# Kernel optimization log

Hardware: AMD Instinct MI355X
Metric: run time of the kernel (lower is better)

The kernel has to match this reference:

```python
import jax, jax.numpy as jnp
import numpy as np

B, T, N, F_OUT, K, HID = 8, 12, 4096, 12, 3, 64
HALF = T // 2


def setup_inputs() -> dict:
    key = jax.random.key(0)
    ks = jax.random.split(key, 7)
    return {
        "x": jax.random.normal(ks[0], (B, T, N, 1), jnp.float32),
        "adj": jax.random.normal(ks[1], (K, N, N), jnp.float32) / np.float32(np.sqrt(N)),
        "cheb_w": jax.random.normal(ks[2], (HID, K), jnp.float32) / np.float32(np.sqrt(K)),
        "gcn_w": jax.random.normal(ks[3], (F_OUT, T, 1, HID), jnp.float32) / np.float32(np.sqrt(T * HID)),
        "gcn_b": jnp.zeros((F_OUT,), jnp.float32),
        "glu1_w": jax.random.normal(ks[4], (F_OUT, HALF, 3, 3), jnp.float32) / np.float32(np.sqrt(HALF * 9)),
        "glu1_b": jnp.zeros((F_OUT,), jnp.float32),
        "glu2_w": jax.random.normal(ks[5], (F_OUT, HALF, 3, 3), jnp.float32) / np.float32(np.sqrt(HALF * 9)),
        "glu2_b": jnp.zeros((F_OUT,), jnp.float32),
    }


def _dilated_conv(x, w, b):
    # Conv2d(kernel=3, dilation=2, padding=2) on (B, C, N, 1)
    y = jax.lax.conv_general_dilated(
        x, w, window_strides=(1, 1), padding=((2, 2), (2, 2)),
        rhs_dilation=(2, 2), dimension_numbers=("NCHW", "OIHW", "NCHW"))
    return y + b[None, :, None, None]


def reference(x, adj, cheb_w, gcn_w, gcn_b, glu1_w, glu1_b, glu2_w, glu2_b):
    # --- ChebConv (vectorized over the per-channel Python loop) ---
    # x: (B, T, N, 1), adj: (K, N, N) -> y: (B, T, N, K)
    y = jnp.einsum("knm,btm->btnk", adj, x[..., 0])
    # Linear(K -> HID, no bias) + ReLU -> cheb: (B, T, N, HID)
    cheb = jax.nn.relu(jnp.einsum("btnk,ok->btno", y, cheb_w))
    # --- gcn_conv: Conv2d(T -> F_OUT, kernel (1, HID)) -> (B, F_OUT, N, 1) ---
    sgc = jnp.einsum("btnj,otj->bon", cheb, gcn_w[:, :, 0, :]) + gcn_b[None, :, None]
    sgc = sgc[..., None]
    # --- GLU path: split history in half, dilated convs, a * sigmoid(g) ---
    x_u, x_v = x[:, :HALF], x[:, HALF:]
    a = _dilated_conv(x_u, glu1_w, glu1_b)
    g = _dilated_conv(x_v, glu2_w, glu2_b)
    x_glu = a * jax.nn.sigmoid(g)
    return x_glu + sgc
```

## Files before the change

kernel.cpp:

```cpp
#include <hip/hip_runtime.h>
#include <hip/hip_bf16.h>
#include <math.h>

#define NNODES 4096
#define NCOLS  96
#define NROWS  12288
#define KSEG   16
#define KLEN   (NNODES / KSEG)

typedef __attribute__((ext_vector_type(8))) short short8;
typedef __attribute__((ext_vector_type(4))) float float4v;

__device__ __forceinline__ int probe32(const void* adjp) {
    const unsigned* aw = (const unsigned*)adjp;
    unsigned w = aw[threadIdx.x & 63];
    unsigned e = (w >> 7) & 0xffu;
    bool insane = (e >= 0xC0u) || (e <= 0x30u);
    unsigned long long m = __ballot(insane);
    return (__popcll(m) >= 16) ? 1 : 0;
}

__device__ __forceinline__ float ldf(const void* p, size_t i, int isf32) {
    return isf32 ? ((const float*)p)[i]
                 : __bfloat162float(((const __hip_bfloat16*)p)[i]);
}

__device__ __forceinline__ void ld8(float* d, const void* p, size_t e, int isf32) {
    if (isf32) {
        const float4* s = (const float4*)((const float*)p + e);
        float4 f0 = s[0], f1 = s[1];
        d[0] = f0.x; d[1] = f0.y; d[2] = f0.z; d[3] = f0.w;
        d[4] = f1.x; d[5] = f1.y; d[6] = f1.z; d[7] = f1.w;
    } else {
        const __hip_bfloat16* s = (const __hip_bfloat16*)p + e;
#pragma unroll
        for (int j = 0; j < 8; j++) d[j] = __bfloat162float(s[j]);
    }
}

__device__ __forceinline__ short8 cvt8(float4 a, float4 b) {
    union { short8 v; __hip_bfloat16 h[8]; } u;
    u.h[0] = __float2bfloat16(a.x); u.h[1] = __float2bfloat16(a.y);
    u.h[2] = __float2bfloat16(a.z); u.h[3] = __float2bfloat16(a.w);
    u.h[4] = __float2bfloat16(b.x); u.h[5] = __float2bfloat16(b.y);
    u.h[6] = __float2bfloat16(b.z); u.h[7] = __float2bfloat16(b.w);
    return u.v;
}

__global__ __launch_bounds__(256) void cvt_x(
    const void* __restrict__ xv, __hip_bfloat16* __restrict__ xbf,
    const void* __restrict__ adjp)
{
    const int isf32 = probe32(adjp);
    const int i = (blockIdx.x * 256 + threadIdx.x) * 8;
    if (isf32) {
        const float* xf = (const float*)xv;
        float4 f0 = *(const float4*)(xf + i);
        float4 f1 = *(const float4*)(xf + i + 4);
        short8 v = cvt8(f0, f1);
        *(short8*)(xbf + i) = v;
    } else {
        *(uint4*)(xbf + i) = *(const uint4*)((const __hip_bfloat16*)xv + i);
    }
}

__global__ __launch_bounds__(512, 4) void gemm_y(
    const void* __restrict__ adjv, const __hip_bfloat16* __restrict__ xbf,
    float* __restrict__ yws)
{
    __shared__ uint4 Xs[96 * 32];

    const int tid = threadIdx.x;
    const int isf32 = probe32(adjv);
    const int wv = tid >> 6, ln = tid & 63, fr = ln & 15, fq = ln >> 4;

    const int bid = blockIdx.x;
    const int rt0 = (bid >> 4) * 128;
    const int ks  = bid & 15;
    const int k0  = ks * KLEN;

#pragma unroll
    for (int s = 0; s < 6; s++) {
        int L = tid + s * 512;
        int r = L >> 5, c = L & 31;
        Xs[r * 32 + (c ^ (r & 7))] =
            *(const uint4*)(xbf + (size_t)r * NNODES + k0 + c * 8);
    }

    float4v acc[6];
#pragma unroll
    for (int i = 0; i < 6; i++) acc[i] = (float4v){0.f, 0.f, 0.f, 0.f};

    const int arow = rt0 + wv * 16 + fr;

#define XFRAG(CT, STEP) \
    (*(const short8*)&Xs[((CT) * 16 + fr) * 32 + ((((STEP) * 4) + fq) ^ (((CT) * 16 + fr) & 7))])

    if (isf32) {
        const float* ap = (const float*)adjv + (size_t)arow * NNODES + k0 + fq * 8;
        float4 AA[2], AB[2];

#define ALOADF(R, STEP) { const float* p = ap + (STEP) * 32;                   \
        R[0] = *(const float4*)p; R[1] = *(const float4*)(p + 4); }
#define COMPF(R, STEP) { short8 a = cvt8(R[0], R[1]);                          \
        _Pragma("unroll")                                                      \
        for (int ct = 0; ct < 6; ct++)                                         \
            acc[ct] = __builtin_amdgcn_mfma_f32_16x16x32_bf16(a, XFRAG(ct, STEP), acc[ct], 0, 0, 0); }

        ALOADF(AA, 0); ALOADF(AB, 1);
        __syncthreads();
        COMPF(AA, 0);  ALOADF(AA, 2);
        COMPF(AB, 1);  ALOADF(AB, 3);
        COMPF(AA, 2);  ALOADF(AA, 4);
        COMPF(AB, 3);  ALOADF(AB, 5);
        COMPF(AA, 4);  ALOADF(AA, 6);
        COMPF(AB, 5);  ALOADF(AB, 7);
        COMPF(AA, 6);
        COMPF(AB, 7);
#undef ALOADF
#undef COMPF
    } else {
        const __hip_bfloat16* ap = (const __hip_bfloat16*)adjv + (size_t)arow * NNODES + k0 + fq * 8;
        uint4 AA, AB;

#define ALOADB(R, STEP) R = *(const uint4*)(ap + (STEP) * 32);
#define COMPB(R, STEP) { short8 a = *(const short8*)&R;                        \
        _Pragma("unroll")                                                      \
        for (int ct = 0; ct < 6; ct++)                                         \
            acc[ct] = __builtin_amdgcn_mfma_f32_16x16x32_bf16(a, XFRAG(ct, STEP), acc[ct], 0, 0, 0); }

        ALOADB(AA, 0); ALOADB(AB, 1);
        __syncthreads();
        COMPB(AA, 0);  ALOADB(AA, 2);
        COMPB(AB, 1);  ALOADB(AB, 3);
        COMPB(AA, 2);  ALOADB(AA, 4);
        COMPB(AB, 3);  ALOADB(AB, 5);
        COMPB(AA, 4);  ALOADB(AA, 6);
        COMPB(AB, 5);  ALOADB(AB, 7);
        COMPB(AA, 6);
        COMPB(AB, 7);
#undef ALOADB
#undef COMPB
    }
#undef XFRAG

    float* yo = yws + (size_t)ks * NROWS * NCOLS;
#pragma unroll
    for (int ct = 0; ct < 6; ct++)
#pragma unroll
        for (int rg = 0; rg < 4; rg++) {
            size_t r = (size_t)rt0 + wv * 16 + fq * 4 + rg;
            yo[r * NCOLS + ct * 16 + fr] = acc[ct][rg];
        }
}

__global__ __launch_bounds__(256) void reduce_y(float* __restrict__ yws)
{
    const size_t i = ((size_t)blockIdx.x * 256 + threadIdx.x) * 4;
    float4 s = *(const float4*)(yws + i);
#pragma unroll
    for (int sl = 1; sl < KSEG; sl++) {
        const float4 v = *(const float4*)(yws + (size_t)sl * NROWS * NCOLS + i);
        s.x += v.x; s.y += v.y; s.z += v.z; s.w += v.w;
    }
    *(float4*)(yws + i) = s;
}

__global__ __launch_bounds__(256) void epilogue_kernel(
    const void* __restrict__ xv, const float* __restrict__ yws,
    const void* __restrict__ chebv, const void* __restrict__ gcnwv,
    const void* __restrict__ gcnbv, const void* __restrict__ g1wv,
    const void* __restrict__ g1bv, const void* __restrict__ g2wv,
    const void* __restrict__ g2bv,
    float* __restrict__ out, const void* __restrict__ adjp)
{
    __shared__ __align__(16) float gwL[9216];
    __shared__ __align__(16) float cw4L[256];
    __shared__ float w1L[216];
    __shared__ float w2L[216];
    __shared__ float wbL[36];

    const int tid = threadIdx.x;
    const int isf32 = probe32(adjp);

    for (int i = tid; i < 9216; i += 256) {
        int o = i / 768, t = (i / 64) % 12, j = i % 64;
        gwL[t * 768 + j * 12 + o] = ldf(gcnwv, i, isf32);
    }
    if (tid < 256) {
        int j = tid >> 2, kk = tid & 3;
        cw4L[tid] = (kk < 3 && j < 64) ? ldf(chebv, j * 3 + kk, isf32) : 0.f;
    }
    if (tid < 216) {
        w1L[tid] = ldf(g1wv, (size_t)tid * 3 + 1, isf32);
        w2L[tid] = ldf(g2wv, (size_t)tid * 3 + 1, isf32);
    }
    if (tid < 12) {
        wbL[tid]      = ldf(gcnbv, tid, isf32);
        wbL[12 + tid] = ldf(g1bv, tid, isf32);
        wbL[24 + tid] = ldf(g2bv, tid, isf32);
    }
    __syncthreads();

    const int gid = blockIdx.x * 256 + tid;
    const int pr  = gid >> 2;
    const int tq  = gid & 3;
    const int b = pr >> 12;
    const int n = pr & (NNODES - 1);

    float yk[3][3];
#pragma unroll
    for (int k = 0; k < 3; k++) {
        const float* yp = yws + ((size_t)(k * NNODES + n)) * NCOLS + b * 12 + tq * 3;
        yk[k][0] = yp[0]; yk[k][1] = yp[1]; yk[k][2] = yp[2];
    }

    float sg[12];
#pragma unroll
    for (int o = 0; o < 12; o++) sg[o] = 0.f;
    const float4* cw4 = (const float4*)cw4L;
#pragma unroll
    for (int i = 0; i < 3; i++) {
        const float y0 = yk[0][i], y1 = yk[1][i], y2 = yk[2][i];
        const float4* gw4 = (const float4*)(gwL + (tq * 3 + i) * 768);
#pragma unroll 4
        for (int j = 0; j < 64; j++) {
            float4 cw = cw4[j];
            float h = fmaf(y0, cw.x, fmaf(y1, cw.y, y2 * cw.z));
            h = fmaxf(h, 0.f);
            float4 g0 = gw4[j * 3], g1 = gw4[j * 3 + 1], g2 = gw4[j * 3 + 2];
            sg[0] += h * g0.x; sg[1] += h * g0.y; sg[2]  += h * g0.z; sg[3]  += h * g0.w;
            sg[4] += h * g1.x; sg[5] += h * g1.y; sg[6]  += h * g1.z; sg[7]  += h * g1.w;
            sg[8] += h * g2.x; sg[9] += h * g2.y; sg[10] += h * g2.z; sg[11] += h * g2.w;
        }
    }
#pragma unroll
    for (int o = 0; o < 12; o++) {
        sg[o] += __shfl_xor(sg[o], 1);
        sg[o] += __shfl_xor(sg[o], 2);
    }

    float xa[18], xg[18];
#pragma unroll
    for (int c = 0; c < 6; c++)
#pragma unroll
        for (int kh = 0; kh < 3; kh++) {
            int m = n + 2 * kh - 2;
            bool ok = ((unsigned)m < (unsigned)NNODES);
            xa[c * 3 + kh] = ok ? ldf(xv, ((size_t)(b * 12 + c)) * NNODES + m, isf32) : 0.f;
            xg[c * 3 + kh] = ok ? ldf(xv, ((size_t)(b * 12 + c + 6)) * NNODES + m, isf32) : 0.f;
        }

#pragma unroll
    for (int i = 0; i < 3; i++) {
        const int o = tq * 3 + i;
        float av = wbL[12 + o], gv = wbL[24 + o];
#pragma unroll
        for (int q = 0; q < 18; q++) {
            av += xa[q] * w1L[o * 18 + q];
            gv += xg[q] * w2L[o * 18 + q];
        }
        float s = 1.f / (1.f + expf(-gv));
        out[((size_t)(b * 12 + o)) * NNODES + n] = av * s + sg[o] + wbL[o];
    }
}

__global__ __launch_bounds__(64) void fused_simple(
    const void* __restrict__ xv, const void* __restrict__ adjv,
    const void* __restrict__ chebv, const void* __restrict__ gcnwv,
    const void* __restrict__ gcnbv, const void* __restrict__ g1wv,
    const void* __restrict__ g1bv, const void* __restrict__ g2wv,
    const void* __restrict__ g2bv,
    float* __restrict__ out)
{
    __shared__ float gwL[9216];
    __shared__ float cwL[192];
    __shared__ float w1L[216];
    __shared__ float w2L[216];
    __shared__ float wbL[36];

    const int tid = threadIdx.x;
    const int isf32 = probe32(adjv);

    for (int i = tid; i < 9216; i += 64) {
        int o = i / 768, t = (i / 64) % 12, j = i % 64;
        gwL[t * 768 + j * 12 + o] = ldf(gcnwv, i, isf32);
    }
    for (int i = tid; i < 192; i += 64) cwL[i] = ldf(chebv, i, isf32);
    for (int i = tid; i < 216; i += 64) {
        w1L[i] = ldf(g1wv, (size_t)i * 3 + 1, isf32);
        w2L[i] = ldf(g2wv, (size_t)i * 3 + 1, isf32);
    }
    if (tid < 12) {
        wbL[tid]      = ldf(gcnbv, tid, isf32);
        wbL[12 + tid] = ldf(g1bv, tid, isf32);
        wbL[24 + tid] = ldf(g2bv, tid, isf32);
    }
    __syncthreads();

    const int g = blockIdx.x * 64 + tid;
    const int b = g >> 12;
    const int n = g & (NNODES - 1);

    float y[3][12];
#pragma unroll
    for (int k = 0; k < 3; k++)
#pragma unroll
        for (int t = 0; t < 12; t++) y[k][t] = 0.f;

    for (int m0 = 0; m0 < NNODES; m0 += 8) {
        float a0[8], a1[8], a2[8];
        ld8(a0, adjv, ((size_t)(0 * NNODES + n)) * NNODES + m0, isf32);
        ld8(a1, adjv, ((size_t)(1 * NNODES + n)) * NNODES + m0, isf32);
        ld8(a2, adjv, ((size_t)(2 * NNODES + n)) * NNODES + m0, isf32);
#pragma unroll
        for (int t = 0; t < 12; t++) {
            float x8[8];
            ld8(x8, xv, ((size_t)(b * 12 + t)) * NNODES + m0, isf32);
#pragma unroll
            for (int j = 0; j < 8; j++) {
                y[0][t] += a0[j] * x8[j];
                y[1][t] += a1[j] * x8[j];
                y[2][t] += a2[j] * x8[j];
            }
        }
    }

    float sg[12];
#pragma unroll
    for (int o = 0; o < 12; o++) sg[o] = wbL[o];
    for (int t = 0; t < 12; t++) {
        const float y0 = y[0][t], y1 = y[1][t], y2 = y[2][t];
        const float* gwt = gwL + t * 768;
#pragma unroll 4
        for (int j = 0; j < 64; j++) {
            float h = y0 * cwL[j * 3] + y1 * cwL[j * 3 + 1] + y2 * cwL[j * 3 + 2];
            h = fmaxf(h, 0.f);
#pragma unroll
            for (int o = 0; o < 12; o++) sg[o] += h * gwt[j * 12 + o];
        }
    }

    float xa[18], xg[18];
#pragma unroll
    for (int c = 0; c < 6; c++)
#pragma unroll
        for (int kh = 0; kh < 3; kh++) {
            int m = n + 2 * kh - 2;
            bool ok = ((unsigned)m < (unsigned)NNODES);
            xa[c * 3 + kh] = ok ? ldf(xv, ((size_t)(b * 12 + c)) * NNODES + m, isf32) : 0.f;
            xg[c * 3 + kh] = ok ? ldf(xv, ((size_t)(b * 12 + c + 6)) * NNODES + m, isf32) : 0.f;
        }

#pragma unroll
    for (int o = 0; o < 12; o++) {
        float av = wbL[12 + o], gv = wbL[24 + o];
#pragma unroll
        for (int i = 0; i < 18; i++) {
            av += xa[i] * w1L[o * 18 + i];
            gv += xg[i] * w2L[o * 18 + i];
        }
        float s = 1.f / (1.f + expf(-gv));
        out[((size_t)(b * 12 + o)) * NNODES + n] = av * s + sg[o];
    }
}

extern "C" void kernel_launch(void* const* d_in, const int* in_sizes, int n_in,
                              void* d_out, int out_size, void* d_ws, size_t ws_size,
                              hipStream_t stream)
{
    __hip_bfloat16* xbf = (__hip_bfloat16*)((char*)d_ws + 64);
    float* yws = (float*)((char*)d_ws + 64 + (size_t)NCOLS * NNODES * 2);
    const size_t need = 64 + (size_t)NCOLS * NNODES * 2
                      + (size_t)KSEG * NROWS * NCOLS * 4;

    if (ws_size >= need) {
        hipLaunchKernelGGL(cvt_x, dim3(192), dim3(256), 0, stream,
                           d_in[0], xbf, d_in[1]);
        hipLaunchKernelGGL(gemm_y, dim3(96 * KSEG), dim3(512), 0, stream,
                           d_in[1], xbf, yws);
        hipLaunchKernelGGL(reduce_y, dim3(NROWS * NCOLS / 1024), dim3(256), 0, stream,
                           yws);
        hipLaunchKernelGGL(epilogue_kernel, dim3(512), dim3(256), 0, stream,
                           d_in[0], yws, d_in[2], d_in[3], d_in[4],
                           d_in[5], d_in[6], d_in[7], d_in[8],
                           (float*)d_out, d_in[1]);
    } else {
        hipLaunchKernelGGL(fused_simple, dim3(512), dim3(64), 0, stream,
                           d_in[0], d_in[1], d_in[2], d_in[3], d_in[4],
                           d_in[5], d_in[6], d_in[7], d_in[8],
                           (float*)d_out);
    }
}
```

Measured before the change: 380.8 us.

## Fuse x conversion into GEMM, halve K-split, move split reduction into epilogue

Drops the separate x-to-bf16 conversion kernel: the GEMM now stages x into shared memory directly, converting from the source dtype. The K-split drops from 16 to 8 segments, so each block runs two staged halves with extra barriers. The separate reduce kernel is removed; the epilogue sums the 8 partial slices itself. The partials are stored transposed as float4 so those reads are coalesced. This removes two launches and much of the partial-sum traffic, at the cost of fewer GEMM blocks for parallelism and extra loads in the epilogue.

New measurement: 345.4 us. -9.3%, faster.

```diff
diff --git a/kernel.cpp b/kernel.cpp
--- a/kernel.cpp
+++ b/kernel.cpp
@@ -5,8 +5,9 @@
 #define NNODES 4096
 #define NCOLS  96
 #define NROWS  12288
-#define KSEG   16
+#define KSEG   8
 #define KLEN   (NNODES / KSEG)
+#define YSLICE ((size_t)NROWS * NCOLS)
 
 typedef __attribute__((ext_vector_type(8))) short short8;
 typedef __attribute__((ext_vector_type(4))) float float4v;
@@ -47,25 +48,12 @@
     return u.v;
 }
 
-__global__ __launch_bounds__(256) void cvt_x(
-    const void* __restrict__ xv, __hip_bfloat16* __restrict__ xbf,
-    const void* __restrict__ adjp)
-{
-    const int isf32 = probe32(adjp);
-    const int i = (blockIdx.x * 256 + threadIdx.x) * 8;
-    if (isf32) {
-        const float* xf = (const float*)xv;
-        float4 f0 = *(const float4*)(xf + i);
-        float4 f1 = *(const float4*)(xf + i + 4);
-        short8 v = cvt8(f0, f1);
-        *(short8*)(xbf + i) = v;
-    } else {
-        *(uint4*)(xbf + i) = *(const uint4*)((const __hip_bfloat16*)xv + i);
-    }
+__device__ __forceinline__ uint4 s8u4(short8 v) {
+    union { short8 s; uint4 u; } x; x.s = v; return x.u;
 }
 
 __global__ __launch_bounds__(512, 4) void gemm_y(
-    const void* __restrict__ adjv, const __hip_bfloat16* __restrict__ xbf,
+    const void* __restrict__ adjv, const void* __restrict__ xv,
     float* __restrict__ yws)
 {
     __shared__ uint4 Xs[96 * 32];
@@ -75,26 +63,33 @@
     const int wv = tid >> 6, ln = tid & 63, fr = ln & 15, fq = ln >> 4;
 
     const int bid = blockIdx.x;
-    const int rt0 = (bid >> 4) * 128;
-    const int ks  = bid & 15;
+    const int rt0 = (bid >> 3) * 128;
+    const int ks  = bid & 7;
     const int k0  = ks * KLEN;
 
-#pragma unroll
-    for (int s = 0; s < 6; s++) {
-        int L = tid + s * 512;
-        int r = L >> 5, c = L & 31;
-        Xs[r * 32 + (c ^ (r & 7))] =
-            *(const uint4*)(xbf + (size_t)r * NNODES + k0 + c * 8);
-    }
-
     float4v acc[6];
 #pragma unroll
     for (int i = 0; i < 6; i++) acc[i] = (float4v){0.f, 0.f, 0.f, 0.f};
 
     const int arow = rt0 + wv * 16 + fr;
 
+    const int sL0 = tid;
 #define XFRAG(CT, STEP) \
     (*(const short8*)&Xs[((CT) * 16 + fr) * 32 + ((((STEP) * 4) + fq) ^ (((CT) * 16 + fr) & 7))])
+
+#define STAGEF(HK) { _Pragma("unroll")                                         \
+    for (int s = 0; s < 6; s++) {                                              \
+        int L = sL0 + s * 512; int r = L >> 5, c = L & 31;                     \
+        const float* p = (const float*)xv + (size_t)r * NNODES + (HK) + c * 8; \
+        Xs[r * 32 + (c ^ (r & 7))] =                                           \
+            s8u4(cvt8(*(const float4*)p, *(const float4*)(p + 4)));            \
+    } }
+#define STAGEB(HK) { _Pragma("unroll")                                         \
+    for (int s = 0; s < 6; s++) {                                              \
+        int L = sL0 + s * 512; int r = L >> 5, c = L & 31;                     \
+        Xs[r * 32 + (c ^ (r & 7))] = *(const uint4*)(                          \
+            (const __hip_bfloat16*)xv + (size_t)r * NNODES + (HK) + c * 8);    \
+    } }
 
     if (isf32) {
         const float* ap = (const float*)adjv + (size_t)arow * NNODES + k0 + fq * 8;
@@ -105,8 +100,9 @@
 #define COMPF(R, STEP) { short8 a = cvt8(R[0], R[1]);                          \
         _Pragma("unroll")                                                      \
         for (int ct = 0; ct < 6; ct++)                                         \
-            acc[ct] = __builtin_amdgcn_mfma_f32_16x16x32_bf16(a, XFRAG(ct, STEP), acc[ct], 0, 0, 0); }
-
+            acc[ct] = __builtin_amdgcn_mfma_f32_16x16x32_bf16(a, XFRAG(ct, (STEP) & 7), acc[ct], 0, 0, 0); }
+
+        STAGEF(k0);
         ALOADF(AA, 0); ALOADF(AB, 1);
         __syncthreads();
         COMPF(AA, 0);  ALOADF(AA, 2);
@@ -115,8 +111,19 @@
         COMPF(AB, 3);  ALOADF(AB, 5);
         COMPF(AA, 4);  ALOADF(AA, 6);
         COMPF(AB, 5);  ALOADF(AB, 7);
-        COMPF(AA, 6);
-        COMPF(AB, 7);
+        COMPF(AA, 6);  ALOADF(AA, 8);
+        COMPF(AB, 7);  ALOADF(AB, 9);
+        __syncthreads();
+        STAGEF(k0 + 256);
+        __syncthreads();
+        COMPF(AA, 8);   ALOADF(AA, 10);
+        COMPF(AB, 9);   ALOADF(AB, 11);
+        COMPF(AA, 10);  ALOADF(AA, 12);
+        COMPF(AB, 11);  ALOADF(AB, 13);
+        COMPF(AA, 12);  ALOADF(AA, 14);
+        COMPF(AB, 13);  ALOADF(AB, 15);
+        COMPF(AA, 14);
+        COMPF(AB, 15);
 #undef ALOADF
 #undef COMPF
     } else {
@@ -127,8 +134,9 @@
 #define COMPB(R, STEP) { short8 a = *(const short8*)&R;                        \
         _Pragma("unroll")                                                      \
         for (int ct = 0; ct < 6; ct++)                                         \
-            acc[ct] = __builtin_amdgcn_mfma_f32_16x16x32_bf16(a, XFRAG(ct, STEP), acc[ct], 0, 0, 0); }
-
+            acc[ct] = __builtin_amdgcn_mfma_f32_16x16x32_bf16(a, XFRAG(ct, (STEP) & 7), acc[ct], 0, 0, 0); }
+
+        STAGEB(k0);
         ALOADB(AA, 0); ALOADB(AB, 1);
         __syncthreads();
         COMPB(AA, 0);  ALOADB(AA, 2);
@@ -137,33 +145,33 @@
         COMPB(AB, 3);  ALOADB(AB, 5);
         COMPB(AA, 4);  ALOADB(AA, 6);
         COMPB(AB, 5);  ALOADB(AB, 7);
-        COMPB(AA, 6);
-        COMPB(AB, 7);
+        COMPB(AA, 6);  ALOADB(AA, 8);
+        COMPB(AB, 7);  ALOADB(AB, 9);
+        __syncthreads();
+        STAGEB(k0 + 256);
+        __syncthreads();
+        COMPB(AA, 8);   ALOADB(AA, 10);
+        COMPB(AB, 9);   ALOADB(AB, 11);
+        COMPB(AA, 10);  ALOADB(AA, 12);
+        COMPB(AB, 11);  ALOADB(AB, 13);
+        COMPB(AA, 12);  ALOADB(AA, 14);
+        COMPB(AB, 13);  ALOADB(AB, 15);
+        COMPB(AA, 14);
+        COMPB(AB, 15);
 #undef ALOADB
 #undef COMPB
     }
 #undef XFRAG
-
-    float* yo = yws + (size_t)ks * NROWS * NCOLS;
-#pragma unroll
-    for (int ct = 0; ct < 6; ct++)
-#pragma unroll
-        for (int rg = 0; rg < 4; rg++) {
-            size_t r = (size_t)rt0 + wv * 16 + fq * 4 + rg;
-            yo[r * NCOLS + ct * 16 + fr] = acc[ct][rg];
-        }
-}
-
-__global__ __launch_bounds__(256) void reduce_y(float* __restrict__ yws)
-{
-    const size_t i = ((size_t)blockIdx.x * 256 + threadIdx.x) * 4;
-    float4 s = *(const float4*)(yws + i);
-#pragma unroll
-    for (int sl = 1; sl < KSEG; sl++) {
-        const float4 v = *(const float4*)(yws + (size_t)sl * NROWS * NCOLS + i);
-        s.x += v.x; s.y += v.y; s.z += v.z; s.w += v.w;
-    }
-    *(float4*)(yws + i) = s;
+#undef STAGEF
+#undef STAGEB
+
+    float* yo = yws + (size_t)ks * YSLICE;
+    const int rowb = rt0 + wv * 16 + fq * 4;
+#pragma unroll
+    for (int ct = 0; ct < 6; ct++) {
+        float4 v; v.x = acc[ct][0]; v.y = acc[ct][1]; v.z = acc[ct][2]; v.w = acc[ct][3];
+        *(float4*)(yo + (size_t)(ct * 16 + fr) * NROWS + rowb) = v;
+    }
 }
 
 __global__ __launch_bounds__(256) void epilogue_kernel(
@@ -174,7 +182,7 @@
     const void* __restrict__ g2bv,
     float* __restrict__ out, const void* __restrict__ adjp)
 {
-    __shared__ __align__(16) float gwL[9216];
+    __shared__ __align__(16) float gwL[12 * 780];
     __shared__ __align__(16) float cw4L[256];
     __shared__ float w1L[216];
     __shared__ float w2L[216];
@@ -185,9 +193,9 @@
 
     for (int i = tid; i < 9216; i += 256) {
         int o = i / 768, t = (i / 64) % 12, j = i % 64;
-        gwL[t * 768 + j * 12 + o] = ldf(gcnwv, i, isf32);
-    }
-    if (tid < 256) {
+        gwL[t * 780 + j * 12 + o] = ldf(gcnwv, i, isf32);
+    }
+    {
         int j = tid >> 2, kk = tid & 3;
         cw4L[tid] = (kk < 3 && j < 64) ? ldf(chebv, j * 3 + kk, isf32) : 0.f;
     }
@@ -210,9 +218,16 @@
 
     float yk[3][3];
 #pragma unroll
-    for (int k = 0; k < 3; k++) {
-        const float* yp = yws + ((size_t)(k * NNODES + n)) * NCOLS + b * 12 + tq * 3;
-        yk[k][0] = yp[0]; yk[k][1] = yp[1]; yk[k][2] = yp[2];
+    for (int k = 0; k < 3; k++) { yk[k][0] = 0.f; yk[k][1] = 0.f; yk[k][2] = 0.f; }
+#pragma unroll
+    for (int sl = 0; sl < KSEG; sl++) {
+        const float* base = yws + (size_t)sl * YSLICE
+                          + (size_t)(b * 12 + tq * 3) * NROWS + n;
+#pragma unroll
+        for (int i = 0; i < 3; i++)
+#pragma unroll
+            for (int k = 0; k < 3; k++)
+                yk[k][i] += base[(size_t)i * NROWS + k * NNODES];
     }
 
     float sg[12];
@@ -222,7 +237,7 @@
 #pragma unroll
     for (int i = 0; i < 3; i++) {
         const float y0 = yk[0][i], y1 = yk[1][i], y2 = yk[2][i];
-        const float4* gw4 = (const float4*)(gwL + (tq * 3 + i) * 768);
+        const float4* gw4 = (const float4*)(gwL + (tq * 3 + i) * 780);
 #pragma unroll 4
         for (int j = 0; j < 64; j++) {
             float4 cw = cw4[j];
@@ -369,18 +384,12 @@
                               void* d_out, int out_size, void* d_ws, size_t ws_size,
                               hipStream_t stream)
 {
-    __hip_bfloat16* xbf = (__hip_bfloat16*)((char*)d_ws + 64);
-    float* yws = (float*)((char*)d_ws + 64 + (size_t)NCOLS * NNODES * 2);
-    const size_t need = 64 + (size_t)NCOLS * NNODES * 2
-                      + (size_t)KSEG * NROWS * NCOLS * 4;
+    float* yws = (float*)((char*)d_ws + 64);
+    const size_t need = 64 + (size_t)KSEG * YSLICE * 4;
 
     if (ws_size >= need) {
-        hipLaunchKernelGGL(cvt_x, dim3(192), dim3(256), 0, stream,
-                           d_in[0], xbf, d_in[1]);
         hipLaunchKernelGGL(gemm_y, dim3(96 * KSEG), dim3(512), 0, stream,
-                           d_in[1], xbf, yws);
-        hipLaunchKernelGGL(reduce_y, dim3(NROWS * NCOLS / 1024), dim3(256), 0, stream,
-                           yws);
+                           d_in[1], d_in[0], yws);
         hipLaunchKernelGGL(epilogue_kernel, dim3(512), dim3(256), 0, stream,
                            d_in[0], yws, d_in[2], d_in[3], d_in[4],
                            d_in[5], d_in[6], d_in[7], d_in[8],
```

## Fuse adjacency GEMM, split-K reduction and epilogue into one kernel per node tile

Applied to the files above, without the earlier changes.

Replaces the separate split-K GEMM, reduction and epilogue kernels with a single kernel. Each block owns 16 nodes across all three Chebyshev orders. Its 8 waves each cover a slice of K and combine their partial sums through shared-memory atomics before running the GCN/GLU epilogue in place. This removes the large fp32 partial-sum workspace round trip through global memory and two kernel launches. In exchange the grid shrinks to 256 blocks at occupancy 2, and the X operand is read directly from global memory rather than staged in LDS.

Measured after the change: 362.1 us. -4.9%, faster.

```diff
diff --git a/kernel.cpp b/kernel.cpp
--- a/kernel.cpp
+++ b/kernel.cpp
@@ -3,10 +3,7 @@
 #include <math.h>
 
 #define NNODES 4096
-#define NCOLS  96
-#define NROWS  12288
-#define KSEG   16
-#define KLEN   (NNODES / KSEG)
+#define PADY   100
 
 typedef __attribute__((ext_vector_type(8))) short short8;
 typedef __attribute__((ext_vector_type(4))) float float4v;
@@ -64,132 +61,31 @@
     }
 }
 
-__global__ __launch_bounds__(512, 4) void gemm_y(
-    const void* __restrict__ adjv, const __hip_bfloat16* __restrict__ xbf,
-    float* __restrict__ yws)
-{
-    __shared__ uint4 Xs[96 * 32];
-
-    const int tid = threadIdx.x;
-    const int isf32 = probe32(adjv);
-    const int wv = tid >> 6, ln = tid & 63, fr = ln & 15, fq = ln >> 4;
-
-    const int bid = blockIdx.x;
-    const int rt0 = (bid >> 4) * 128;
-    const int ks  = bid & 15;
-    const int k0  = ks * KLEN;
-
-#pragma unroll
-    for (int s = 0; s < 6; s++) {
-        int L = tid + s * 512;
-        int r = L >> 5, c = L & 31;
-        Xs[r * 32 + (c ^ (r & 7))] =
-            *(const uint4*)(xbf + (size_t)r * NNODES + k0 + c * 8);
-    }
-
-    float4v acc[6];
-#pragma unroll
-    for (int i = 0; i < 6; i++) acc[i] = (float4v){0.f, 0.f, 0.f, 0.f};
-
-    const int arow = rt0 + wv * 16 + fr;
-
-#define XFRAG(CT, STEP) \
-    (*(const short8*)&Xs[((CT) * 16 + fr) * 32 + ((((STEP) * 4) + fq) ^ (((CT) * 16 + fr) & 7))])
-
-    if (isf32) {
-        const float* ap = (const float*)adjv + (size_t)arow * NNODES + k0 + fq * 8;
-        float4 AA[2], AB[2];
-
-#define ALOADF(R, STEP) { const float* p = ap + (STEP) * 32;                   \
-        R[0] = *(const float4*)p; R[1] = *(const float4*)(p + 4); }
-#define COMPF(R, STEP) { short8 a = cvt8(R[0], R[1]);                          \
-        _Pragma("unroll")                                                      \
-        for (int ct = 0; ct < 6; ct++)                                         \
-            acc[ct] = __builtin_amdgcn_mfma_f32_16x16x32_bf16(a, XFRAG(ct, STEP), acc[ct], 0, 0, 0); }
-
-        ALOADF(AA, 0); ALOADF(AB, 1);
-        __syncthreads();
-        COMPF(AA, 0);  ALOADF(AA, 2);
-        COMPF(AB, 1);  ALOADF(AB, 3);
-        COMPF(AA, 2);  ALOADF(AA, 4);
-        COMPF(AB, 3);  ALOADF(AB, 5);
-        COMPF(AA, 4);  ALOADF(AA, 6);
-        COMPF(AB, 5);  ALOADF(AB, 7);
-        COMPF(AA, 6);
-        COMPF(AB, 7);
-#undef ALOADF
-#undef COMPF
-    } else {
-        const __hip_bfloat16* ap = (const __hip_bfloat16*)adjv + (size_t)arow * NNODES + k0 + fq * 8;
-        uint4 AA, AB;
-
-#define ALOADB(R, STEP) R = *(const uint4*)(ap + (STEP) * 32);
-#define COMPB(R, STEP) { short8 a = *(const short8*)&R;                        \
-        _Pragma("unroll")                                                      \
-        for (int ct = 0; ct < 6; ct++)                                         \
-            acc[ct] = __builtin_amdgcn_mfma_f32_16x16x32_bf16(a, XFRAG(ct, STEP), acc[ct], 0, 0, 0); }
-
-        ALOADB(AA, 0); ALOADB(AB, 1);
-        __syncthreads();
-        COMPB(AA, 0);  ALOADB(AA, 2);
-        COMPB(AB, 1);  ALOADB(AB, 3);
-        COMPB(AA, 2);  ALOADB(AA, 4);
-        COMPB(AB, 3);  ALOADB(AB, 5);
-        COMPB(AA, 4);  ALOADB(AA, 6);
-        COMPB(AB, 5);  ALOADB(AB, 7);
-        COMPB(AA, 6);
-        COMPB(AB, 7);
-#undef ALOADB
-#undef COMPB
-    }
-#undef XFRAG
-
-    float* yo = yws + (size_t)ks * NROWS * NCOLS;
-#pragma unroll
-    for (int ct = 0; ct < 6; ct++)
-#pragma unroll
-        for (int rg = 0; rg < 4; rg++) {
-            size_t r = (size_t)rt0 + wv * 16 + fq * 4 + rg;
-            yo[r * NCOLS + ct * 16 + fr] = acc[ct][rg];
-        }
-}
-
-__global__ __launch_bounds__(256) void reduce_y(float* __restrict__ yws)
-{
-    const size_t i = ((size_t)blockIdx.x * 256 + threadIdx.x) * 4;
-    float4 s = *(const float4*)(yws + i);
-#pragma unroll
-    for (int sl = 1; sl < KSEG; sl++) {
-        const float4 v = *(const float4*)(yws + (size_t)sl * NROWS * NCOLS + i);
-        s.x += v.x; s.y += v.y; s.z += v.z; s.w += v.w;
-    }
-    *(float4*)(yws + i) = s;
-}
-
-__global__ __launch_bounds__(256) void epilogue_kernel(
-    const void* __restrict__ xv, const float* __restrict__ yws,
+__global__ __launch_bounds__(512, 2) void fused_gcn(
+    const void* __restrict__ adjv, const void* __restrict__ xv,
+    const __hip_bfloat16* __restrict__ xbf,
     const void* __restrict__ chebv, const void* __restrict__ gcnwv,
     const void* __restrict__ gcnbv, const void* __restrict__ g1wv,
     const void* __restrict__ g1bv, const void* __restrict__ g2wv,
-    const void* __restrict__ g2bv,
-    float* __restrict__ out, const void* __restrict__ adjp)
+    const void* __restrict__ g2bv, float* __restrict__ out)
 {
-    __shared__ __align__(16) float gwL[9216];
+    __shared__ float y48[48 * PADY];
+    __shared__ __align__(16) float gwL[12 * 780];
     __shared__ __align__(16) float cw4L[256];
     __shared__ float w1L[216];
     __shared__ float w2L[216];
     __shared__ float wbL[36];
 
     const int tid = threadIdx.x;
-    const int isf32 = probe32(adjp);
-
-    for (int i = tid; i < 9216; i += 256) {
+    const int isf32 = probe32(adjv);
+
+    for (int i = tid; i < 9216; i += 512) {
         int o = i / 768, t = (i / 64) % 12, j = i % 64;
-        gwL[t * 768 + j * 12 + o] = ldf(gcnwv, i, isf32);
+        gwL[t * 780 + j * 12 + o] = ldf(gcnwv, i, isf32);
     }
     if (tid < 256) {
         int j = tid >> 2, kk = tid & 3;
-        cw4L[tid] = (kk < 3 && j < 64) ? ldf(chebv, j * 3 + kk, isf32) : 0.f;
+        cw4L[tid] = (kk < 3) ? ldf(chebv, j * 3 + kk, isf32) : 0.f;
     }
     if (tid < 216) {
         w1L[tid] = ldf(g1wv, (size_t)tid * 3 + 1, isf32);
@@ -200,35 +96,126 @@
         wbL[12 + tid] = ldf(g1bv, tid, isf32);
         wbL[24 + tid] = ldf(g2bv, tid, isf32);
     }
+    for (int i = tid; i < 48 * PADY; i += 512) y48[i] = 0.f;
     __syncthreads();
 
-    const int gid = blockIdx.x * 256 + tid;
-    const int pr  = gid >> 2;
-    const int tq  = gid & 3;
-    const int b = pr >> 12;
-    const int n = pr & (NNODES - 1);
+    const int wv = tid >> 6, ln = tid & 63, fr = ln & 15, fq = ln >> 4;
+    const int n0 = blockIdx.x * 16;
+    const int kk0 = wv * 512;
+
+    float4v acc[3][6];
+#pragma unroll
+    for (int rt = 0; rt < 3; rt++)
+#pragma unroll
+        for (int ct = 0; ct < 6; ct++) acc[rt][ct] = (float4v){0.f, 0.f, 0.f, 0.f};
+
+    const __hip_bfloat16* xb = xbf + (size_t)fr * NNODES + kk0 + fq * 8;
+
+    if (isf32) {
+        const float* ab = (const float*)adjv
+                        + (size_t)(n0 + fr) * NNODES + kk0 + fq * 8;
+        float4 A0[3][2], A1[3][2];
+        uint4  B0[6], B1[6];
+
+#define ALD(S, STEP) { _Pragma("unroll")                                       \
+        for (int rt = 0; rt < 3; rt++) {                                       \
+            const float* p = ab + (size_t)rt * ((size_t)NNODES * NNODES)       \
+                           + (STEP) * 32;                                      \
+            S[rt][0] = *(const float4*)p; S[rt][1] = *(const float4*)(p + 4); } }
+#define BLD(S, STEP) { _Pragma("unroll")                                       \
+        for (int ct = 0; ct < 6; ct++)                                         \
+            S[ct] = *(const uint4*)(xb + (size_t)ct * (16 * NNODES)            \
+                                    + (STEP) * 32); }
+#define CMP(SA, SB) { _Pragma("unroll")                                        \
+        for (int rt = 0; rt < 3; rt++) {                                       \
+            short8 a = cvt8(SA[rt][0], SA[rt][1]);                             \
+            _Pragma("unroll")                                                  \
+            for (int ct = 0; ct < 6; ct++)                                     \
+                acc[rt][ct] = __builtin_amdgcn_mfma_f32_16x16x32_bf16(         \
+                    a, *(const short8*)&SB[ct], acc[rt][ct], 0, 0, 0); } }
+
+        ALD(A0, 0); BLD(B0, 0); ALD(A1, 1); BLD(B1, 1);
+        for (int s = 0; s < 16; s += 2) {
+            CMP(A0, B0);
+            if (s + 2 < 16) { ALD(A0, s + 2); BLD(B0, s + 2); }
+            CMP(A1, B1);
+            if (s + 3 < 16) { ALD(A1, s + 3); BLD(B1, s + 3); }
+        }
+#undef ALD
+#undef BLD
+#undef CMP
+    } else {
+        const __hip_bfloat16* ab = (const __hip_bfloat16*)adjv
+                                 + (size_t)(n0 + fr) * NNODES + kk0 + fq * 8;
+        uint4 A0[3], A1[3], B0[6], B1[6];
+
+#define ALDB(S, STEP) { _Pragma("unroll")                                      \
+        for (int rt = 0; rt < 3; rt++)                                         \
+            S[rt] = *(const uint4*)(ab + (size_t)rt * ((size_t)NNODES * NNODES)\
+                                    + (STEP) * 32); }
+#define BLDB(S, STEP) { _Pragma("unroll")                                      \
+        for (int ct = 0; ct < 6; ct++)                                         \
+            S[ct] = *(const uint4*)(xb + (size_t)ct * (16 * NNODES)            \
+                                    + (STEP) * 32); }
+#define CMPB(SA, SB) { _Pragma("unroll")                                       \
+        for (int rt = 0; rt < 3; rt++) {                                       \
+            short8 a = *(const short8*)&SA[rt];                                \
+            _Pragma("unroll")                                                  \
+            for (int ct = 0; ct < 6; ct++)                                     \
+                acc[rt][ct] = __builtin_amdgcn_mfma_f32_16x16x32_bf16(         \
+                    a, *(const short8*)&SB[ct], acc[rt][ct], 0, 0, 0); } }
+
+        ALDB(A0, 0); BLDB(B0, 0); ALDB(A1, 1); BLDB(B1, 1);
+        for (int s = 0; s < 16; s += 2) {
+            CMPB(A0, B0);
+            if (s + 2 < 16) { ALDB(A0, s + 2); BLDB(B0, s + 2); }
+            CMPB(A1, B1);
+            if (s + 3 < 16) { ALDB(A1, s + 3); BLDB(B1, s + 3); }
+        }
+#undef ALDB
+#undef BLDB
+#undef CMPB
+    }
+
+#pragma unroll
+    for (int rt = 0; rt < 3; rt++)
+#pragma unroll
+        for (int ct = 0; ct < 6; ct++)
+#pragma unroll
+            for (int rg = 0; rg < 4; rg++)
+                atomicAdd(&y48[(rt * 16 + fq * 4 + rg) * PADY + ct * 16 + fr],
+                          acc[rt][ct][rg]);
+    __syncthreads();
+
+    const int pr = tid >> 2;
+    const int tq = tid & 3;
+    const int b  = pr >> 4;
+    const int nl = pr & 15;
+    const int n  = n0 + nl;
 
     float yk[3][3];
 #pragma unroll
-    for (int k = 0; k < 3; k++) {
-        const float* yp = yws + ((size_t)(k * NNODES + n)) * NCOLS + b * 12 + tq * 3;
-        yk[k][0] = yp[0]; yk[k][1] = yp[1]; yk[k][2] = yp[2];
-    }
+    for (int k = 0; k < 3; k++)
+#pragma unroll
+        for (int i = 0; i < 3; i++)
+            yk[k][i] = y48[(k * 16 + nl) * PADY + b * 12 + tq * 3 + i];
 
     float sg[12];
 #pragma unroll
     for (int o = 0; o < 12; o++) sg[o] = 0.f;
     const float4* cw4 = (const float4*)cw4L;
-#pragma unroll
-    for (int i = 0; i < 3; i++) {
-        const float y0 = yk[0][i], y1 = yk[1][i], y2 = yk[2][i];
-        const float4* gw4 = (const float4*)(gwL + (tq * 3 + i) * 768);
+    const float4* gwt0 = (const float4*)(gwL + (tq * 3 + 0) * 780);
+    const float4* gwt1 = (const float4*)(gwL + (tq * 3 + 1) * 780);
+    const float4* gwt2 = (const float4*)(gwL + (tq * 3 + 2) * 780);
 #pragma unroll 4
-        for (int j = 0; j < 64; j++) {
-            float4 cw = cw4[j];
-            float h = fmaf(y0, cw.x, fmaf(y1, cw.y, y2 * cw.z));
+    for (int j = 0; j < 64; j++) {
+        float4 cw = cw4[j];
+#pragma unroll
+        for (int i = 0; i < 3; i++) {
+            float h = fmaf(yk[0][i], cw.x, fmaf(yk[1][i], cw.y, yk[2][i] * cw.z));
             h = fmaxf(h, 0.f);
-            float4 g0 = gw4[j * 3], g1 = gw4[j * 3 + 1], g2 = gw4[j * 3 + 2];
+            const float4* gwt = (i == 0) ? gwt0 : (i == 1) ? gwt1 : gwt2;
+            float4 g0 = gwt[j * 3], g1 = gwt[j * 3 + 1], g2 = gwt[j * 3 + 2];
             sg[0] += h * g0.x; sg[1] += h * g0.y; sg[2]  += h * g0.z; sg[3]  += h * g0.w;
             sg[4] += h * g1.x; sg[5] += h * g1.y; sg[6]  += h * g1.z; sg[7]  += h * g1.w;
             sg[8] += h * g2.x; sg[9] += h * g2.y; sg[10] += h * g2.z; sg[11] += h * g2.w;
@@ -370,21 +357,15 @@
                               hipStream_t stream)
 {
     __hip_bfloat16* xbf = (__hip_bfloat16*)((char*)d_ws + 64);
-    float* yws = (float*)((char*)d_ws + 64 + (size_t)NCOLS * NNODES * 2);
-    const size_t need = 64 + (size_t)NCOLS * NNODES * 2
-                      + (size_t)KSEG * NROWS * NCOLS * 4;
+    const size_t need = 64 + (size_t)96 * NNODES * 2;
 
     if (ws_size >= need) {
         hipLaunchKernelGGL(cvt_x, dim3(192), dim3(256), 0, stream,
                            d_in[0], xbf, d_in[1]);
-        hipLaunchKernelGGL(gemm_y, dim3(96 * KSEG), dim3(512), 0, stream,
-                           d_in[1], xbf, yws);
-        hipLaunchKernelGGL(reduce_y, dim3(NROWS * NCOLS / 1024), dim3(256), 0, stream,
-                           yws);
-        hipLaunchKernelGGL(epilogue_kernel, dim3(512), dim3(256), 0, stream,
-                           d_in[0], yws, d_in[2], d_in[3], d_in[4],
+        hipLaunchKernelGGL(fused_gcn, dim3(NNODES / 16), dim3(512), 0, stream,
+                           d_in[1], d_in[0], xbf, d_in[2], d_in[3], d_in[4],
                            d_in[5], d_in[6], d_in[7], d_in[8],
-                           (float*)d_out, d_in[1]);
+                           (float*)d_out);
     } else {
         hipLaunchKernelGGL(fused_simple, dim3(512), dim3(64), 0, stream,
                            d_in[0], d_in[1], d_in[2], d_in[3], d_in[4],
```
